# Kernel optimization log

Hardware: AMD Instinct MI355X
Metric: run time of the kernel (lower is better)

The kernel has to match this reference:

```python
import jax, jax.numpy as jnp
import numpy as np

N_NODES = 16  # superpixels per sample (gcn1 nodes)


def setup_inputs() -> dict:
    key = jax.random.key(0)
    ks = jax.random.split(key, 10)
    B, Cin, H, W = 32, 64, 112, 112
    Cout, H2, W2 = 128, 56, 56
    E = 64
    inp = {
        "B_for": jax.random.normal(ks[0], (B, Cin, H, W), jnp.float32),
        "B_fon": jax.random.normal(ks[1], (B, Cout, H2, W2), jnp.float32),
        "seg": jax.random.randint(ks[2], (B, H, W), 0, N_NODES, jnp.int32),
        "src": jax.random.randint(ks[3], (B, E), 0, N_NODES, jnp.int32),
        "dst": jax.random.randint(ks[4], (B, E), 0, N_NODES, jnp.int32),
        "conv_w": jax.random.normal(ks[5], (1, Cin), jnp.float32) * 0.1,
        "conv_b": jnp.zeros((1,), jnp.float32),
        "W1": jax.random.normal(ks[6], (4, 32), jnp.float32) * 0.3,
        "b1": jnp.zeros((32,), jnp.float32),
        "W2": jax.random.normal(ks[7], (32, Cout), jnp.float32) * 0.15,
        "b2": jnp.zeros((Cout,), jnp.float32),
        "fc_w": jax.random.normal(ks[8], (1, N_NODES), jnp.float32) * 0.2,
        "fc_b": jnp.zeros((1,), jnp.float32),
    }
    return inp


def _superpixel_features(L, seg):
    # L: [B,1,H,W] intensity; seg: [B,H,W] labels in [0, N_NODES)
    B, _, H, W = L.shape
    ids = (seg + jnp.arange(B, dtype=seg.dtype)[:, None, None] * N_NODES).reshape(-1)
    Lf = L[:, 0].reshape(-1)
    ones = jnp.ones_like(Lf)
    rows = jnp.broadcast_to(jnp.arange(H, dtype=L.dtype)[None, :, None], (B, H, W)).reshape(-1)
    cols = jnp.broadcast_to(jnp.arange(W, dtype=L.dtype)[None, None, :], (B, H, W)).reshape(-1)
    nseg = B * N_NODES
    cnt = jax.ops.segment_sum(ones, ids, num_segments=nseg)
    s_r = jax.ops.segment_sum(rows, ids, num_segments=nseg)
    s_c = jax.ops.segment_sum(cols, ids, num_segments=nseg)
    s_i = jax.ops.segment_sum(Lf, ids, num_segments=nseg)
    cnt_safe = jnp.maximum(cnt, 1.0)
    feats = jnp.stack([s_r / cnt_safe, s_c / cnt_safe, s_i / cnt_safe, cnt], axis=-1)
    feats = feats.reshape(B, N_NODES, 4)
    # normalize mean_intensity and area columns: (x - mean) / (std + 1), unbiased std
    sub = feats[..., 2:]
    mu = sub.mean(axis=1, keepdims=True)
    sd = jnp.std(sub, axis=1, keepdims=True, ddof=1)
    return jnp.concatenate([feats[..., :2], (sub - mu) / (sd + 1.0)], axis=-1)


def _graph_conv(A, nrm, X, Wt, bt):
    # DGL GraphConv, norm='both': D^{-1/2} A D^{-1/2} X W + b
    agg = jnp.einsum('bij,bjf->bif', A, nrm[..., None] * X)
    return nrm[..., None] * agg @ Wt + bt


def reference(B_for, B_fon, seg, src, dst, conv_w, conv_b, W1, b1, W2, b2, fc_w, fc_b):
    B = B_for.shape[0]
    # 1x1 conv -> single-channel intensity map L
    L = jnp.einsum('bchw,oc->bohw', B_for, conv_w) + conv_b[None, :, None, None]
    X = _superpixel_features(L, seg)  # [B, N, 4]
    # symmetric adjacency from edge list
    bidx = jnp.arange(B)[:, None]
    A = jnp.zeros((B, N_NODES, N_NODES), B_for.dtype)
    A = A.at[bidx, src, dst].set(1.0)
    A = A.at[bidx, dst, src].set(1.0)
    nrm = jnp.clip(A.sum(-1), 1.0, None) ** -0.5
    h1 = jax.nn.relu(_graph_conv(A, nrm, X, W1, b1))   # [B, N, 32]
    h2 = jax.nn.relu(_graph_conv(A, nrm, h1, W2, b2))  # [B, N, 128]
    # fc over nodes: Linear(N -> 1) applied to h2.T  => [B, 128]
    G = jnp.einsum('bnf,n->bf', h2, fc_w[0]) + fc_b[0]
    # broadcast-modulate dense CNN features
    return G[:, :, None, None] * B_fon
```

## Files before the change

kernel.cpp:

```cpp
#include <hip/hip_runtime.h>

#define NN 16
constexpr int BB = 32, CIN = 64, HH = 112, WW = 112;
constexpr int HWC = HH * WW;
constexpr int COUT = 128, HW2 = 56 * 56;
constexpr int NE = 64;
constexpr int NQ = HWC / 4;
constexpr int QPB = 64;
constexpr int BPI = NQ / QPB;
constexpr int PF4 = COUT * HW2 / 4;
constexpr int SBPB = 25;

__global__ __launch_bounds__(256) void k_conv_seg(
    const float* __restrict__ Bfor, const int* __restrict__ seg,
    const float* __restrict__ convw, float* __restrict__ part)
{
    __shared__ float w[CIN];
    __shared__ float ps[4][QPB * 5];
    __shared__ float acc[8 * 80];
    const int tid = threadIdx.x;
    const int b   = blockIdx.x / BPI;
    const int blk = blockIdx.x % BPI;
    const int cg  = tid >> 6;
    const int l   = tid & 63;

    if (tid < CIN) w[tid] = convw[tid];
    for (int i = tid; i < 8 * 80; i += 256) acc[i] = 0.f;
    __syncthreads();

    const int p = (blk * QPB + l) * 4;
    const float* base = Bfor + (size_t)b * CIN * HWC + (size_t)(cg * 16) * HWC + p;

    float4 s = make_float4(0.f, 0.f, 0.f, 0.f);
    #pragma unroll
    for (int cc = 0; cc < 16; ++cc) {
        const float4 v = *reinterpret_cast<const float4*>(base + (size_t)cc * HWC);
        const float wc = w[cg * 16 + cc];
        s.x = fmaf(v.x, wc, s.x);
        s.y = fmaf(v.y, wc, s.y);
        s.z = fmaf(v.z, wc, s.z);
        s.w = fmaf(v.w, wc, s.w);
    }
    ps[cg][l * 5 + 0] = s.x;
    ps[cg][l * 5 + 1] = s.y;
    ps[cg][l * 5 + 2] = s.z;
    ps[cg][l * 5 + 3] = s.w;
    __syncthreads();

    {
        const int q  = tid >> 2, px = tid & 3;
        const float v = ps[0][q * 5 + px] + ps[1][q * 5 + px]
                      + ps[2][q * 5 + px] + ps[3][q * 5 + px];
        const int pp  = blk * 256 + tid;
        const int sgv = seg[(size_t)b * HWC + pp];
        const float row = (float)(pp / WW);
        const float col = (float)(pp % WW);
        const int k = tid & 7;
        float* a = &acc[k * 80 + sgv * 5];
        atomicAdd(a + 0, row);
        atomicAdd(a + 1, col);
        atomicAdd(a + 2, v);
        atomicAdd(a + 3, 1.f);
    }
    __syncthreads();

    if (tid < NN * 4) {
        const int node = tid >> 2, st = tid & 3;
        float v = 0.f;
        #pragma unroll
        for (int k = 0; k < 8; ++k) v += acc[k * 80 + node * 5 + st];
        part[((b * BPI + blk) * NN + node) * 4 + st] = v;
    }
}

__global__ __launch_bounds__(256) void k_graph_scale(
    const float* __restrict__ part, const int* __restrict__ src,
    const int* __restrict__ dst,  const float* __restrict__ convb,
    const float* __restrict__ W1, const float* __restrict__ b1,
    const float* __restrict__ W2, const float* __restrict__ b2,
    const float* __restrict__ fcw, const float* __restrict__ fcb,
    const float* __restrict__ Bfon, float* __restrict__ out)
{
    const int b    = blockIdx.x / SBPB;
    const int blkb = blockIdx.x % SBPB;
    const int tid  = threadIdx.x;

    __shared__ float X[NN][4];
    __shared__ float A[NN][NN];
    __shared__ float nrm[NN];
    __shared__ float h1s[NN][32];
    __shared__ float agg[NN][32];
    __shared__ float pred[4][64];
    __shared__ float gpart[2][COUT];
    __shared__ float Gs[COUT];

    {
        const int id = tid & 63, chunk = tid >> 6;
        float v = 0.f;
        const int k0 = chunk * 13, k1e = (k0 + 13 < BPI) ? k0 + 13 : BPI;
        for (int k = k0; k < k1e; ++k) v += part[(size_t)(b * BPI + k) * 64 + id];
        pred[chunk][id] = v;
    }
    for (int i = tid; i < NN * NN; i += 256) ((float*)A)[i] = 0.f;
    __syncthreads();

    if (tid < 64) {
        const int node = tid >> 2, st = tid & 3;
        X[node][st] = pred[0][tid] + pred[1][tid] + pred[2][tid] + pred[3][tid];
    }
    __syncthreads();

    if (tid < NN) {
        const float cnt = X[tid][3];
        const float cs  = fmaxf(cnt, 1.f);
        X[tid][0] = X[tid][0] / cs;
        X[tid][1] = X[tid][1] / cs;
        X[tid][2] = (X[tid][2] + cnt * convb[0]) / cs;
    }
    __syncthreads();

    if (tid < 2) {
        const int c = 2 + tid;
        float mu = 0.f;
        for (int i = 0; i < NN; ++i) mu += X[i][c];
        mu *= (1.f / NN);
        float var = 0.f;
        for (int i = 0; i < NN; ++i) { const float d = X[i][c] - mu; var = fmaf(d, d, var); }
        var *= (1.f / (NN - 1));
        const float inv = 1.f / (sqrtf(var) + 1.f);
        for (int i = 0; i < NN; ++i) X[i][c] = (X[i][c] - mu) * inv;
    }
    if (tid >= 64 && tid < 64 + NE) {
        const int e = tid - 64;
        const int s = src[b * NE + e], d = dst[b * NE + e];
        A[s][d] = 1.f;
        A[d][s] = 1.f;
    }
    __syncthreads();

    if (tid < NN) {
        float rs = 0.f;
        for (int j = 0; j < NN; ++j) rs += A[tid][j];
        nrm[tid] = 1.f / sqrtf(fmaxf(rs, 1.f));
    }
    __syncthreads();

    if (tid < NN * 4) {
        const int i = tid >> 2, k = tid & 3;
        float s = 0.f;
        for (int j = 0; j < NN; ++j) s = fmaf(A[i][j] * nrm[j], X[j][k], s);
        agg[i][k] = s;
    }
    __syncthreads();

    for (int t = tid; t < NN * 32; t += 256) {
        const int i = t >> 5, f = t & 31;
        float s = 0.f;
        #pragma unroll
        for (int k = 0; k < 4; ++k) s = fmaf(agg[i][k], W1[k * 32 + f], s);
        h1s[i][f] = fmaxf(fmaf(nrm[i], s, b1[f]), 0.f);
    }
    __syncthreads();

    for (int t = tid; t < NN * 32; t += 256) {
        const int i = t >> 5, k = t & 31;
        float s = 0.f;
        for (int j = 0; j < NN; ++j) s = fmaf(A[i][j] * nrm[j], h1s[j][k], s);
        agg[i][k] = s;
    }
    __syncthreads();

    {
        const int f = tid & 127, half = tid >> 7;
        float g = 0.f;
        const float bf = b2[f];
        for (int i = half * 8; i < half * 8 + 8; ++i) {
            float s = 0.f;
            #pragma unroll
            for (int k = 0; k < 32; ++k) s = fmaf(agg[i][k], W2[k * COUT + f], s);
            g = fmaf(fcw[i], fmaxf(fmaf(nrm[i], s, bf), 0.f), g);
        }
        gpart[half][f] = g;
    }
    __syncthreads();
    if (tid < COUT) Gs[tid] = gpart[0][tid] + gpart[1][tid] + fcb[0];
    __syncthreads();

    const float4* bf4 = reinterpret_cast<const float4*>(Bfon) + (size_t)b * PF4;
    float4*       ob4 = reinterpret_cast<float4*>(out)        + (size_t)b * PF4;
    for (int t = blkb * 256 + tid; t < PF4; t += SBPB * 256) {
        const float4 v = bf4[t];
        const float  g = Gs[t / (HW2 / 4)];
        ob4[t] = make_float4(v.x * g, v.y * g, v.z * g, v.w * g);
    }
}

extern "C" void kernel_launch(void* const* d_in, const int* in_sizes, int n_in,
                              void* d_out, int out_size, void* d_ws, size_t ws_size,
                              hipStream_t stream)
{
    const float* Bfor  = (const float*)d_in[0];
    const float* Bfon  = (const float*)d_in[1];
    const int*   seg   = (const int*)d_in[2];
    const int*   src   = (const int*)d_in[3];
    const int*   dst   = (const int*)d_in[4];
    const float* convw = (const float*)d_in[5];
    const float* convb = (const float*)d_in[6];
    const float* W1    = (const float*)d_in[7];
    const float* b1    = (const float*)d_in[8];
    const float* W2    = (const float*)d_in[9];
    const float* b2    = (const float*)d_in[10];
    const float* fcw   = (const float*)d_in[11];
    const float* fcb   = (const float*)d_in[12];

    float* part = (float*)d_ws;
    float* out  = (float*)d_out;

    k_conv_seg<<<BB * BPI, 256, 0, stream>>>(Bfor, seg, convw, part);
    k_graph_scale<<<BB * SBPB, 256, 0, stream>>>(part, src, dst, convb,
                                                 W1, b1, W2, b2, fcw, fcb,
                                                 Bfon, out);
}
```

Baseline: 50.83 us.

## Split graph and scale kernels; prefetch B_fon into cache during conv pass

The fused graph+scale kernel becomes a small per-sample graph kernel that writes G, followed by a separate fully parallel scale kernel. The conv/segment kernel now also streams all of B_fon and reduces it into a dummy output so the data is warm in the cache before the scale pass. The seg load is hoisted ahead of the channel reduction. In exchange the step adds an extra launch and extra read traffic in the first kernel, and it depends on B_fon staying resident in the last-level cache.

```diff
diff --git a/kernel.cpp b/kernel.cpp
--- a/kernel.cpp
+++ b/kernel.cpp
@@ -9,24 +9,30 @@
 constexpr int QPB = 64;
 constexpr int BPI = NQ / QPB;
 constexpr int PF4 = COUT * HW2 / 4;
-constexpr int SBPB = 25;
+constexpr int NB1 = BB * BPI;
+constexpr int N4  = BB * PF4;
+constexpr int WPB = N4 / NB1 / 256;
 
 __global__ __launch_bounds__(256) void k_conv_seg(
     const float* __restrict__ Bfor, const int* __restrict__ seg,
-    const float* __restrict__ convw, float* __restrict__ part)
+    const float* __restrict__ convw, const float* __restrict__ Bfon,
+    float* __restrict__ part, float* __restrict__ dump)
 {
     __shared__ float w[CIN];
     __shared__ float ps[4][QPB * 5];
     __shared__ float acc[8 * 80];
     const int tid = threadIdx.x;
-    const int b   = blockIdx.x / BPI;
-    const int blk = blockIdx.x % BPI;
+    const int bid = blockIdx.x;
+    const int b   = bid / BPI;
+    const int blk = bid % BPI;
     const int cg  = tid >> 6;
     const int l   = tid & 63;
 
+    const int pp  = blk * 256 + tid;
+    const int sgv = seg[(size_t)b * HWC + pp];
+
     if (tid < CIN) w[tid] = convw[tid];
     for (int i = tid; i < 8 * 80; i += 256) acc[i] = 0.f;
-    __syncthreads();
 
     const int p = (blk * QPB + l) * 4;
     const float* base = Bfor + (size_t)b * CIN * HWC + (size_t)(cg * 16) * HWC + p;
@@ -41,18 +47,25 @@
         s.z = fmaf(v.z, wc, s.z);
         s.w = fmaf(v.w, wc, s.w);
     }
+    __syncthreads();
     ps[cg][l * 5 + 0] = s.x;
     ps[cg][l * 5 + 1] = s.y;
     ps[cg][l * 5 + 2] = s.z;
     ps[cg][l * 5 + 3] = s.w;
+
+    const float4* wf = reinterpret_cast<const float4*>(Bfon) + (size_t)bid * 2048 + tid;
+    float4 wa = make_float4(0.f, 0.f, 0.f, 0.f);
+    #pragma unroll
+    for (int j = 0; j < WPB; ++j) {
+        const float4 v = wf[j * 256];
+        wa.x += v.x; wa.y += v.y; wa.z += v.z; wa.w += v.w;
+    }
     __syncthreads();
 
     {
         const int q  = tid >> 2, px = tid & 3;
         const float v = ps[0][q * 5 + px] + ps[1][q * 5 + px]
                       + ps[2][q * 5 + px] + ps[3][q * 5 + px];
-        const int pp  = blk * 256 + tid;
-        const int sgv = seg[(size_t)b * HWC + pp];
         const float row = (float)(pp / WW);
         const float col = (float)(pp % WW);
         const int k = tid & 7;
@@ -71,19 +84,21 @@
         for (int k = 0; k < 8; ++k) v += acc[k * 80 + node * 5 + st];
         part[((b * BPI + blk) * NN + node) * 4 + st] = v;
     }
-}
-
-__global__ __launch_bounds__(256) void k_graph_scale(
+    if ((tid & 63) == 0) {
+        const float t0 = wa.x + wa.y + wa.z + wa.w;
+        dump[bid * 4 + cg] = t0;
+    }
+}
+
+__global__ __launch_bounds__(256) void k_graph(
     const float* __restrict__ part, const int* __restrict__ src,
     const int* __restrict__ dst,  const float* __restrict__ convb,
     const float* __restrict__ W1, const float* __restrict__ b1,
     const float* __restrict__ W2, const float* __restrict__ b2,
     const float* __restrict__ fcw, const float* __restrict__ fcb,
-    const float* __restrict__ Bfon, float* __restrict__ out)
-{
-    const int b    = blockIdx.x / SBPB;
-    const int blkb = blockIdx.x % SBPB;
-    const int tid  = threadIdx.x;
+    float* __restrict__ G)
+{
+    const int b = blockIdx.x, tid = threadIdx.x;
 
     __shared__ float X[NN][4];
     __shared__ float A[NN][NN];
@@ -92,7 +107,6 @@
     __shared__ float agg[NN][32];
     __shared__ float pred[4][64];
     __shared__ float gpart[2][COUT];
-    __shared__ float Gs[COUT];
 
     {
         const int id = tid & 63, chunk = tid >> 6;
@@ -183,14 +197,21 @@
         gpart[half][f] = g;
     }
     __syncthreads();
-    if (tid < COUT) Gs[tid] = gpart[0][tid] + gpart[1][tid] + fcb[0];
-    __syncthreads();
-
-    const float4* bf4 = reinterpret_cast<const float4*>(Bfon) + (size_t)b * PF4;
-    float4*       ob4 = reinterpret_cast<float4*>(out)        + (size_t)b * PF4;
-    for (int t = blkb * 256 + tid; t < PF4; t += SBPB * 256) {
+    if (tid < COUT) G[b * COUT + tid] = gpart[0][tid] + gpart[1][tid] + fcb[0];
+}
+
+__global__ __launch_bounds__(256) void k_scale(
+    const float* __restrict__ Bfon, const float* __restrict__ G,
+    float* __restrict__ out)
+{
+    const int t0 = blockIdx.x * 256 + threadIdx.x;
+    const float4* bf4 = reinterpret_cast<const float4*>(Bfon);
+    float4*       ob4 = reinterpret_cast<float4*>(out);
+    #pragma unroll
+    for (int j = 0; j < WPB; ++j) {
+        const int t = t0 + j * (NB1 * 256);
         const float4 v = bf4[t];
-        const float  g = Gs[t / (HW2 / 4)];
+        const float  g = G[t / (HW2 / 4)];
         ob4[t] = make_float4(v.x * g, v.y * g, v.z * g, v.w * g);
     }
 }
@@ -214,10 +235,12 @@
     const float* fcb   = (const float*)d_in[12];
 
     float* part = (float*)d_ws;
+    float* G    = part + BB * BPI * NN * 4;
+    float* dump = G + BB * COUT;
     float* out  = (float*)d_out;
 
-    k_conv_seg<<<BB * BPI, 256, 0, stream>>>(Bfor, seg, convw, part);
-    k_graph_scale<<<BB * SBPB, 256, 0, stream>>>(part, src, dst, convb,
-                                                 W1, b1, W2, b2, fcw, fcb,
-                                                 Bfon, out);
-}
+    k_conv_seg<<<NB1, 256, 0, stream>>>(Bfor, seg, convw, Bfon, part, dump);
+    k_graph<<<BB, 256, 0, stream>>>(part, src, dst, convb,
+                                    W1, b1, W2, b2, fcw, fcb, G);
+    k_scale<<<NB1, 256, 0, stream>>>(Bfon, G, out);
+}
```

New measurement: 56.99 us. 1.12x slower.

## Give each conv thread all 64 channels for four pixels, cutting blocks to 13 per image

Applied to the files above, without the earlier changes.

The 1x1 conv kernel is restructured so each thread reduces all 64 input channels for its own 4 pixels, loading 16 float4s at a time to keep more loads in flight. This removes the cross-warp shared-memory partial-sum step and one barrier. Blocks per image drop from 49 to 13, so the graph kernel sums 13 partials directly without its chunked pre-reduction. In exchange there are far fewer blocks (416) to cover the GPU, more registers per thread, and four times as many shared atomics per thread.

```diff
diff --git a/kernel.cpp b/kernel.cpp
--- a/kernel.cpp
+++ b/kernel.cpp
@@ -6,8 +6,7 @@
 constexpr int COUT = 128, HW2 = 56 * 56;
 constexpr int NE = 64;
 constexpr int NQ = HWC / 4;
-constexpr int QPB = 64;
-constexpr int BPI = NQ / QPB;
+constexpr int BPI = 13;
 constexpr int PF4 = COUT * HW2 / 4;
 constexpr int SBPB = 25;
 
@@ -16,51 +15,58 @@
     const float* __restrict__ convw, float* __restrict__ part)
 {
     __shared__ float w[CIN];
-    __shared__ float ps[4][QPB * 5];
     __shared__ float acc[8 * 80];
     const int tid = threadIdx.x;
     const int b   = blockIdx.x / BPI;
     const int blk = blockIdx.x % BPI;
-    const int cg  = tid >> 6;
-    const int l   = tid & 63;
 
     if (tid < CIN) w[tid] = convw[tid];
     for (int i = tid; i < 8 * 80; i += 256) acc[i] = 0.f;
     __syncthreads();
 
-    const int p = (blk * QPB + l) * 4;
-    const float* base = Bfor + (size_t)b * CIN * HWC + (size_t)(cg * 16) * HWC + p;
-
-    float4 s = make_float4(0.f, 0.f, 0.f, 0.f);
-    #pragma unroll
-    for (int cc = 0; cc < 16; ++cc) {
-        const float4 v = *reinterpret_cast<const float4*>(base + (size_t)cc * HWC);
-        const float wc = w[cg * 16 + cc];
-        s.x = fmaf(v.x, wc, s.x);
-        s.y = fmaf(v.y, wc, s.y);
-        s.z = fmaf(v.z, wc, s.z);
-        s.w = fmaf(v.w, wc, s.w);
-    }
-    ps[cg][l * 5 + 0] = s.x;
-    ps[cg][l * 5 + 1] = s.y;
-    ps[cg][l * 5 + 2] = s.z;
-    ps[cg][l * 5 + 3] = s.w;
-    __syncthreads();
-
-    {
-        const int q  = tid >> 2, px = tid & 3;
-        const float v = ps[0][q * 5 + px] + ps[1][q * 5 + px]
-                      + ps[2][q * 5 + px] + ps[3][q * 5 + px];
-        const int pp  = blk * 256 + tid;
-        const int sgv = seg[(size_t)b * HWC + pp];
-        const float row = (float)(pp / WW);
-        const float col = (float)(pp % WW);
+    const int q = blk * 256 + tid;
+    if (q < NQ) {
+        const int p = q * 4;
+        const float* base = Bfor + (size_t)b * CIN * HWC + p;
+
+        float4 s = make_float4(0.f, 0.f, 0.f, 0.f);
+        #pragma unroll
+        for (int cb = 0; cb < 4; ++cb) {
+            float4 v[16];
+            #pragma unroll
+            for (int j = 0; j < 16; ++j)
+                v[j] = *reinterpret_cast<const float4*>(base + (size_t)(cb * 16 + j) * HWC);
+            #pragma unroll
+            for (int j = 0; j < 16; ++j) {
+                const float wc = w[cb * 16 + j];
+                s.x = fmaf(v[j].x, wc, s.x);
+                s.y = fmaf(v[j].y, wc, s.y);
+                s.z = fmaf(v[j].z, wc, s.z);
+                s.w = fmaf(v[j].w, wc, s.w);
+            }
+        }
+
+        const int4 sg = *reinterpret_cast<const int4*>(seg + (size_t)b * HWC + p);
+        const float row  = (float)(p / WW);
+        const float col0 = (float)(p % WW);
         const int k = tid & 7;
-        float* a = &acc[k * 80 + sgv * 5];
-        atomicAdd(a + 0, row);
-        atomicAdd(a + 1, col);
-        atomicAdd(a + 2, v);
-        atomicAdd(a + 3, 1.f);
+        float* a0 = &acc[k * 80];
+        atomicAdd(a0 + sg.x * 5 + 0, row);
+        atomicAdd(a0 + sg.x * 5 + 1, col0);
+        atomicAdd(a0 + sg.x * 5 + 2, s.x);
+        atomicAdd(a0 + sg.x * 5 + 3, 1.f);
+        atomicAdd(a0 + sg.y * 5 + 0, row);
+        atomicAdd(a0 + sg.y * 5 + 1, col0 + 1.f);
+        atomicAdd(a0 + sg.y * 5 + 2, s.y);
+        atomicAdd(a0 + sg.y * 5 + 3, 1.f);
+        atomicAdd(a0 + sg.z * 5 + 0, row);
+        atomicAdd(a0 + sg.z * 5 + 1, col0 + 2.f);
+        atomicAdd(a0 + sg.z * 5 + 2, s.z);
+        atomicAdd(a0 + sg.z * 5 + 3, 1.f);
+        atomicAdd(a0 + sg.w * 5 + 0, row);
+        atomicAdd(a0 + sg.w * 5 + 1, col0 + 3.f);
+        atomicAdd(a0 + sg.w * 5 + 2, s.w);
+        atomicAdd(a0 + sg.w * 5 + 3, 1.f);
     }
     __syncthreads();
 
@@ -90,24 +96,17 @@
     __shared__ float nrm[NN];
     __shared__ float h1s[NN][32];
     __shared__ float agg[NN][32];
-    __shared__ float pred[4][64];
     __shared__ float gpart[2][COUT];
     __shared__ float Gs[COUT];
 
-    {
-        const int id = tid & 63, chunk = tid >> 6;
-        float v = 0.f;
-        const int k0 = chunk * 13, k1e = (k0 + 13 < BPI) ? k0 + 13 : BPI;
-        for (int k = k0; k < k1e; ++k) v += part[(size_t)(b * BPI + k) * 64 + id];
-        pred[chunk][id] = v;
-    }
-    for (int i = tid; i < NN * NN; i += 256) ((float*)A)[i] = 0.f;
-    __syncthreads();
-
     if (tid < 64) {
         const int node = tid >> 2, st = tid & 3;
-        X[node][st] = pred[0][tid] + pred[1][tid] + pred[2][tid] + pred[3][tid];
-    }
+        float v = 0.f;
+        #pragma unroll
+        for (int k = 0; k < BPI; ++k) v += part[((b * BPI + k) * NN + node) * 4 + st];
+        X[node][st] = v;
+    }
+    for (int i = tid; i < NN * NN; i += 256) ((float*)A)[i] = 0.f;
     __syncthreads();
 
     if (tid < NN) {
```

Measured after the change: 51.40 us. No clear change (+1.1%).
